# Performance work log

Hardware: AMD Instinct MI355X
Metric: run time of the kernel (lower is better)

The kernel has to match this reference:

```python
import jax, jax.numpy as jnp
import numpy as np

N = 8192
FEAT = 200
SEG = FEAT // 4  # 50
OUT = 300


def setup_inputs() -> dict:
    key = jax.random.key(0)
    ks = jax.random.split(key, 10)
    x = jax.random.normal(ks[0], (N, FEAT), dtype=jnp.float32)
    # row-normalized-ish dense adjacencies so activations stay O(1)
    A_S = jax.random.uniform(ks[1], (N, N), dtype=jnp.float32) / N
    A_F = jax.random.uniform(ks[2], (N, N), dtype=jnp.float32) / N
    gcn_W = jax.random.normal(ks[3], (SEG, SEG), dtype=jnp.float32) / np.sqrt(SEG)
    gcn_b = jnp.zeros((SEG,), dtype=jnp.float32)
    # 12 forget gates: order s1,s2,s3,f1,f2,f3,s1b,s2b,s3b,f1b,f2b,f3b
    gates_W = jax.random.normal(ks[4], (12, 2 * SEG, SEG), dtype=jnp.float32)
    gates_b = jax.random.normal(ks[5], (12, SEG), dtype=jnp.float32)
    proj_W = jax.random.normal(ks[6], (8 * SEG, OUT), dtype=jnp.float32) / np.sqrt(8 * SEG)
    proj_b = jnp.zeros((OUT,), dtype=jnp.float32)
    return {"x": x, "A_S": A_S, "A_F": A_F, "gcn_W": gcn_W, "gcn_b": gcn_b,
            "gates_W": gates_W, "gates_b": gates_b, "proj_W": proj_W, "proj_b": proj_b}


def _lgfm(x, A_S, A_F, gcn_W, gcn_b, gates_W, gates_b, proj_W, proj_b):
    seg = x.shape[1] // 4

    def gcn(h, A):
        # Kipf GraphConvolution: relu(A @ (h @ W) + b); dropout inactive (eval)
        return jax.nn.relu(A @ (h @ gcn_W) + gcn_b)

    def gate(i, h1, h2):
        a = jax.nn.sigmoid(jnp.concatenate([h1, h2], axis=1) @ gates_W[i] + gates_b[i])
        return a * h1

    GS1, GS2, GS3, GF1, GF2, GF3 = 0, 1, 2, 3, 4, 5
    GS1B, GS2B, GS3B, GF1B, GF2B, GF3B = 6, 7, 8, 9, 10, 11

    x1, x2, x3, x4 = x[:, :seg], x[:, seg:2 * seg], x[:, 2 * seg:3 * seg], x[:, 3 * seg:]

    # forward branch (F path then S gating)
    t1_XF1 = x1 + gcn(x1, A_F)
    t1_XS1 = gcn(x1, A_S)
    t1_XF2 = 0.2 * t1_XS1 + 0.8 * gcn(t1_XF1, A_F)
    t2_XF1 = x2 + gcn(x2, A_F)
    t2_XS1 = gcn(x2, A_S)
    t2_XS1 = t2_XS1 + gate(GS1, t1_XS1, t2_XS1)
    t2_XF2 = 0.2 * t2_XS1 + 0.8 * gcn(t2_XF1, A_F)
    t2_XF2 = gate(GF1, t1_XF2, t2_XF2) + t2_XF2
    t3_XF1 = 0.2 * x3 + 0.8 * gcn(x3, A_F)
    t3_XS1 = gcn(x3, A_S)
    t3_XS1 = t3_XS1 + gate(GS2, t2_XS1, t3_XS1)
    t3_XF2 = 0.2 * t3_XS1 + 0.8 * gcn(t3_XF1, A_F)
    t3_XF2 = gate(GF2, t2_XF2, t3_XF2) + t3_XF2
    t4_XF1 = x4 + gcn(x4, A_F)
    t4_XS1 = gcn(x4, A_S)
    t4_XS1 = t4_XS1 + gate(GS3, t3_XS1, t4_XS1)
    t4_XF2 = 0.2 * t4_XS1 + 0.8 * gcn(t4_XF1, A_F)
    t4_XF2 = gate(GF3, t3_XF2, t4_XF2) + t4_XF2

    # mirrored branch (S path then F gating)
    t1_XS1b = x1 + gcn(x1, A_S)
    t1_XF1b = gcn(x1, A_F)
    t1_XS2 = 0.2 * t1_XF1b + 0.8 * gcn(t1_XS1b, A_S)
    t2_XS1b = x2 + gcn(x2, A_S)
    t2_XF1b = gcn(x2, A_F)
    t2_XF1b = t2_XF1b + gate(GF1B, t1_XF1b, t2_XF1b)
    t2_XS2 = 0.2 * t2_XF1b + 0.8 * gcn(t2_XS1b, A_S)
    t2_XS2 = gate(GS1B, t1_XS2, t2_XS2) + t2_XS2
    t3_XS1b = 0.2 * x3 + 0.8 * gcn(x3, A_S)
    t3_XF1b = gcn(x3, A_F)
    t3_XF1b = t3_XF1b + gate(GF2B, t2_XF1b, t3_XF1b)
    t3_XS2 = 0.2 * t3_XF1b + 0.8 * gcn(t3_XS1b, A_S)
    t3_XS2 = gate(GS2B, t2_XS2, t3_XS2) + t3_XS2
    t4_XS1b = x4 + gcn(x4, A_S)
    t4_XF1b = gcn(x4, A_F)
    t4_XF1b = t4_XF1b + gate(GF3B, t3_XF1b, t4_XF1b)
    t4_XS2 = 0.2 * t4_XF1b + 0.8 * gcn(t4_XS1b, A_S)
    t4_XS2 = gate(GS3B, t3_XS2, t4_XS2) + t4_XS2

    h_L = jnp.concatenate([t1_XF2, t1_XS2, t2_XF2, t2_XS2,
                           t3_XF2, t3_XS2, t4_XF2, t4_XS2], axis=1)
    return h_L @ proj_W + proj_b


def reference(x, A_S, A_F, gcn_W, gcn_b, gates_W, gates_b, proj_W, proj_b):
    return _lgfm(x, A_S, A_F, gcn_W, gcn_b, gates_W, gates_b, proj_W, proj_b)
```

## Files before the change

kernel.cpp:

```cpp
#include <hip/hip_runtime.h>
#include <math.h>

typedef float float4v __attribute__((ext_vector_type(4)));
typedef __attribute__((ext_vector_type(4))) float f32x4;
typedef __attribute__((ext_vector_type(8))) short short8v;
typedef __attribute__((ext_vector_type(8))) unsigned short ushort8v;

#define NROW 8192
#define FEAT 200
#define OUTC 300
#define ZLD  256
#define HLK  448
#define HLN  384

__device__ __forceinline__ unsigned short f2bf(float x) {
  unsigned u = __float_as_uint(x);
  return (unsigned short)((u + 0x7fffu + ((u >> 16) & 1u)) >> 16);
}

__global__ __launch_bounds__(256) void zmul_t_kernel(
    const float* __restrict__ x, const float* __restrict__ W,
    unsigned short* __restrict__ Zt) {
  __shared__ float Ws[2500];
  __shared__ float hs[16][200];
  __shared__ float zbuf[16][256];
  int t = threadIdx.x;
  int r0 = blockIdx.x * 16;
  for (int i = t; i < 2500; i += 256) Ws[i] = W[i];
  for (int i = t; i < 16 * FEAT; i += 256)
    hs[0][i] = x[(size_t)r0 * FEAT + i];
  __syncthreads();
  for (int i = t; i < 16 * 256; i += 256) {
    int row = i >> 8, j = i & 255;
    float acc = 0.f;
    if (j < FEAT) {
      int s = j / 50, jj = j % 50;
      const float* hrow = &hs[row][s * 50];
      #pragma unroll 5
      for (int k = 0; k < 50; ++k) acc += hrow[k] * Ws[k * 50 + jj];
    }
    zbuf[row][j] = acc;
  }
  __syncthreads();
  unsigned int* Ztu = (unsigned int*)Zt;
  for (int i = t; i < 256 * 8; i += 256) {
    int j = i >> 3, w2 = i & 7;
    unsigned int lo = f2bf(zbuf[2 * w2][j]);
    unsigned int hi = f2bf(zbuf[2 * w2 + 1][j]);
    Ztu[((j * NROW + r0) >> 1) + w2] = lo | (hi << 16);
  }
}

__global__ __launch_bounds__(256, 2) void gemm_cvt_spill_kernel(
    const float* __restrict__ AF, const float* __restrict__ AS,
    const unsigned short* __restrict__ ZtF,
    const unsigned short* __restrict__ ZtS,
    float* __restrict__ Cpart,
    unsigned short* __restrict__ AbF_o, unsigned short* __restrict__ AbS_o) {
  int d = blockIdx.x;
  int L = (d & 7) * 64 + (d >> 3);
  int mat = L & 1;
  int ks  = (L >> 1) & 1;
  int cb  = (L >> 2) & 1;
  int rb  = L >> 3;

  const float* __restrict__ A = mat ? AS : AF;
  const unsigned short* __restrict__ Zt = mat ? ZtS : ZtF;
  unsigned short* __restrict__ Abo = mat ? AbS_o : AbF_o;

  int t = threadIdx.x;
  int lane = t & 63, wv = t >> 6;
  int row0 = rb * 128, n0 = cb * 128, k0 = ks * 4096;

  __shared__ short As[2][128 * 64];
  __shared__ short Bs[2][128 * 64];

  int srcAf[4], dstA[4];
  #pragma unroll
  for (int i = 0; i < 4; ++i) {
    int cc = i * 256 + t;
    int m = cc >> 3, s = cc & 7;
    srcAf[i] = (row0 + m) * NROW + s * 8;
    dstA[i] = m * 64 + ((s ^ (m & 7)) * 8);
  }
  int srcB[4], ldsDstB[4];
  #pragma unroll
  for (int i = 0; i < 4; ++i) {
    int c = i * 256 + t;
    int m = c >> 3, sl = c & 7;
    srcB[i] = (n0 + m) * NROW + ((sl ^ (m & 7)) * 8);
    ldsDstB[i] = (i * 256 + wv * 64) * 8;
  }

  f32x4 ar0[4], ar1[4];

#define STAGE_B(buf, kt)                                                              \
  {                                                                                   \
    _Pragma("unroll")                                                                 \
    for (int i = 0; i < 4; ++i)                                                       \
      __builtin_amdgcn_global_load_lds(                                               \
          (const __attribute__((address_space(1))) void*)(Zt + srcB[i] + (kt)),       \
          (__attribute__((address_space(3))) void*)(&Bs[buf][ldsDstB[i]]), 16, 0, 0); \
  }
#define LOAD_A(kt)                                         \
  {                                                        \
    _Pragma("unroll")                                      \
    for (int i = 0; i < 4; ++i) {                          \
      ar0[i] = *(const f32x4*)&A[srcAf[i] + (kt)];         \
      ar1[i] = *(const f32x4*)&A[srcAf[i] + (kt) + 4];     \
    }                                                      \
  }
#define WRITE_A(buf, kt)                                                                \
  {                                                                                     \
    _Pragma("unroll")                                                                   \
    for (int i = 0; i < 4; ++i) {                                                       \
      unsigned u0_, u1_, u2_, u3_;                                                      \
      asm("v_cvt_pk_bf16_f32 %0, %1, %2" : "=v"(u0_) : "v"(ar0[i][0]), "v"(ar0[i][1]));\
      asm("v_cvt_pk_bf16_f32 %0, %1, %2" : "=v"(u1_) : "v"(ar0[i][2]), "v"(ar0[i][3]));\
      asm("v_cvt_pk_bf16_f32 %0, %1, %2" : "=v"(u2_) : "v"(ar1[i][0]), "v"(ar1[i][1]));\
      asm("v_cvt_pk_bf16_f32 %0, %1, %2" : "=v"(u3_) : "v"(ar1[i][2]), "v"(ar1[i][3]));\
      union { unsigned u[4]; short8v v; } pk_;                                          \
      pk_.u[0] = u0_; pk_.u[1] = u1_; pk_.u[2] = u2_; pk_.u[3] = u3_;                   \
      *(short8v*)&As[buf][dstA[i]] = pk_.v;                                             \
      if (cb == 0) *(short8v*)&Abo[(size_t)srcAf[i] + (kt)] = pk_.v;                    \
    }                                                                                   \
  }

  f32x4 acc[4][4];
  #pragma unroll
  for (int i = 0; i < 4; ++i)
    #pragma unroll
    for (int j = 0; j < 4; ++j) acc[i][j] = (f32x4)0.f;

  int m0 = (wv >> 1) * 64, n0w = (wv & 1) * 64;
  int l15 = lane & 15, l4 = lane >> 4;

  int cur = 0;
  LOAD_A(k0)
  STAGE_B(0, k0)
  WRITE_A(0, k0)
  __syncthreads();

  for (int it = 0; it < 64; ++it) {
    if (it + 1 < 64) {
      STAGE_B(cur ^ 1, k0 + (it + 1) * 64)
      LOAD_A(k0 + (it + 1) * 64)
    }

    #pragma unroll
    for (int kk = 0; kk < 2; ++kk) {
      int slot = kk * 4 + l4;
      short8v a[4], b[4];
      #pragma unroll
      for (int i = 0; i < 4; ++i) {
        int m = m0 + i * 16 + l15;
        a[i] = *(const short8v*)&As[cur][m * 64 + ((slot ^ (m & 7)) * 8)];
        int n = n0w + i * 16 + l15;
        b[i] = *(const short8v*)&Bs[cur][n * 64 + ((slot ^ (n & 7)) * 8)];
      }
      #pragma unroll
      for (int i = 0; i < 4; ++i)
        #pragma unroll
        for (int j = 0; j < 4; ++j)
          acc[i][j] = __builtin_amdgcn_mfma_f32_16x16x32_bf16(a[i], b[j], acc[i][j], 0, 0, 0);
    }

    if (it + 1 < 64) WRITE_A(cur ^ 1, k0 + (it + 1) * 64)
    __syncthreads();
    cur ^= 1;
  }
#undef STAGE_B
#undef LOAD_A
#undef WRITE_A

  int s = mat * 2 + ks;
  #pragma unroll
  for (int i = 0; i < 4; ++i) {
    #pragma unroll
    for (int j = 0; j < 4; ++j) {
      int c = n0 + n0w + j * 16 + l15;
      #pragma unroll
      for (int q = 0; q < 4; ++q) {
        int r = row0 + m0 + i * 16 + l4 * 4 + q;
        Cpart[((size_t)(s * NROW + r) << 8) + c] = acc[i][j][q];
      }
    }
  }
}

__global__ __launch_bounds__(256, 2) void gemm_pair_kernel(
    const unsigned short* __restrict__ AbF,
    const unsigned short* __restrict__ AbS,
    const unsigned short* __restrict__ ZtF,
    const unsigned short* __restrict__ ZtS,
    float* __restrict__ Cpart) {
  int d = blockIdx.x;
  int L = (d & 7) * 64 + (d >> 3);
  int mat = L & 1;
  int ks  = (L >> 1) & 1;
  int cb  = (L >> 2) & 1;
  int rb  = L >> 3;

  const unsigned short* __restrict__ Ab = mat ? AbS : AbF;
  const unsigned short* __restrict__ Zt = mat ? ZtS : ZtF;

  int t = threadIdx.x;
  int lane = t & 63, wv = t >> 6;
  int row0 = rb * 128, n0 = cb * 128, k0 = ks * 4096;

  __shared__ short As[2][128 * 64];
  __shared__ short Bs[2][128 * 64];

  int srcA[4], srcB[4], ldsDst[4];
  #pragma unroll
  for (int i = 0; i < 4; ++i) {
    int c = i * 256 + t;
    int m = c >> 3, sl = c & 7;
    int sw = ((sl ^ (m & 7)) * 8);
    srcA[i] = (row0 + m) * NROW + sw;
    srcB[i] = (n0 + m) * NROW + sw;
    ldsDst[i] = (i * 256 + wv * 64) * 8;
  }

#define STAGE_TILE(buf, kt)                                                          \
  {                                                                                  \
    _Pragma("unroll")                                                                \
    for (int i = 0; i < 4; ++i) {                                                    \
      __builtin_amdgcn_global_load_lds(                                              \
          (const __attribute__((address_space(1))) void*)(Ab + srcA[i] + (kt)),      \
          (__attribute__((address_space(3))) void*)(&As[buf][ldsDst[i]]), 16, 0, 0); \
      __builtin_amdgcn_global_load_lds(                                              \
          (const __attribute__((address_space(1))) void*)(Zt + srcB[i] + (kt)),      \
          (__attribute__((address_space(3))) void*)(&Bs[buf][ldsDst[i]]), 16, 0, 0); \
    }                                                                                \
  }

  f32x4 acc[4][4];
  #pragma unroll
  for (int i = 0; i < 4; ++i)
    #pragma unroll
    for (int j = 0; j < 4; ++j) acc[i][j] = (f32x4)0.f;

  int m0 = (wv >> 1) * 64, n0w = (wv & 1) * 64;
  int l15 = lane & 15, l4 = lane >> 4;

  int cur = 0;
  STAGE_TILE(0, k0)
  __syncthreads();

  for (int it = 0; it < 64; ++it) {
    if (it + 1 < 64) STAGE_TILE(cur ^ 1, k0 + (it + 1) * 64)

    #pragma unroll
    for (int kk = 0; kk < 2; ++kk) {
      int slot = kk * 4 + l4;
      short8v a[4], b[4];
      #pragma unroll
      for (int i = 0; i < 4; ++i) {
        int m = m0 + i * 16 + l15;
        a[i] = *(const short8v*)&As[cur][m * 64 + ((slot ^ (m & 7)) * 8)];
        int n = n0w + i * 16 + l15;
        b[i] = *(const short8v*)&Bs[cur][n * 64 + ((slot ^ (n & 7)) * 8)];
      }
      #pragma unroll
      for (int i = 0; i < 4; ++i)
        #pragma unroll
        for (int j = 0; j < 4; ++j)
          acc[i][j] = __builtin_amdgcn_mfma_f32_16x16x32_bf16(a[i], b[j], acc[i][j], 0, 0, 0);
    }
    __syncthreads();
    cur ^= 1;
  }
#undef STAGE_TILE

  int s = mat * 2 + ks;
  #pragma unroll
  for (int i = 0; i < 4; ++i) {
    #pragma unroll
    for (int j = 0; j < 4; ++j) {
      int c = n0 + n0w + j * 16 + l15;
      #pragma unroll
      for (int q = 0; q < 4; ++q) {
        int r = row0 + m0 + i * 16 + l4 * 4 + q;
        Cpart[((size_t)(s * NROW + r) << 8) + c] = acc[i][j][q];
      }
    }
  }
}

__global__ __launch_bounds__(256) void reduce_zmul_kernel(
    const float* __restrict__ Cpart, const float* __restrict__ bias,
    const float* __restrict__ x, const float* __restrict__ W,
    float* __restrict__ GF0, float* __restrict__ GS0,
    unsigned short* __restrict__ ZtF, unsigned short* __restrict__ ZtS) {
  __shared__ float Ws[2500];
  __shared__ float hs[16][200];
  __shared__ float zbuf[16][256];
  int t = threadIdx.x;
  int r0 = blockIdx.x * 16;
  int w = t >> 6, j = t & 63;
  bool act = j < 50;
  int rbase = r0 + w * 4;
  for (int i = t; i < 2500; i += 256) Ws[i] = W[i];

  const float alpha[4] = {1.f, 1.f, 0.2f, 1.f};
  const float beta[4]  = {1.f, 1.f, 0.8f, 1.f};
  float gf[4][4], gs[4][4];
  if (act) {
    float bv = bias[j];
    #pragma unroll
    for (int r = 0; r < 4; ++r)
      #pragma unroll
      for (int s = 0; s < 4; ++s) {
        int c = s * 50 + j;
        size_t base = (((size_t)(rbase + r)) << 8) + c;
        float vF = Cpart[base] + Cpart[base + (size_t)NROW * 256];
        float vS = Cpart[base + (size_t)2 * NROW * 256] + Cpart[base + (size_t)3 * NROW * 256];
        gf[r][s] = fmaxf(vF + bv, 0.f);
        gs[r][s] = fmaxf(vS + bv, 0.f);
        GF0[(size_t)(rbase + r) * FEAT + c] = gf[r][s];
        GS0[(size_t)(rbase + r) * FEAT + c] = gs[r][s];
      }
    #pragma unroll
    for (int r = 0; r < 4; ++r)
      #pragma unroll
      for (int s = 0; s < 4; ++s)
        hs[w * 4 + r][s * 50 + j] =
            alpha[s] * x[(size_t)(rbase + r) * FEAT + s * 50 + j] + beta[s] * gf[r][s];
  }
  __syncthreads();
  for (int i = t; i < 16 * 256; i += 256) {
    int row = i >> 8, jj = i & 255;
    float acc = 0.f;
    if (jj < FEAT) {
      int s = jj / 50, j2 = jj % 50;
      const float* hrow = &hs[row][s * 50];
      #pragma unroll 5
      for (int k = 0; k < 50; ++k) acc += hrow[k] * Ws[k * 50 + j2];
    }
    zbuf[row][jj] = acc;
  }
  __syncthreads();
  {
    unsigned int* Ztu = (unsigned int*)ZtF;
    for (int i = t; i < 256 * 8; i += 256) {
      int j2 = i >> 3, w2 = i & 7;
      unsigned int lo = f2bf(zbuf[2 * w2][j2]);
      unsigned int hi = f2bf(zbuf[2 * w2 + 1][j2]);
      Ztu[((j2 * NROW + r0) >> 1) + w2] = lo | (hi << 16);
    }
  }
  if (act) {
    #pragma unroll
    for (int r = 0; r < 4; ++r)
      #pragma unroll
      for (int s = 0; s < 4; ++s)
        hs[w * 4 + r][s * 50 + j] =
            alpha[s] * x[(size_t)(rbase + r) * FEAT + s * 50 + j] + beta[s] * gs[r][s];
  }
  __syncthreads();
  for (int i = t; i < 16 * 256; i += 256) {
    int row = i >> 8, jj = i & 255;
    float acc = 0.f;
    if (jj < FEAT) {
      int s = jj / 50, j2 = jj % 50;
      const float* hrow = &hs[row][s * 50];
      #pragma unroll 5
      for (int k = 0; k < 50; ++k) acc += hrow[k] * Ws[k * 50 + j2];
    }
    zbuf[row][jj] = acc;
  }
  __syncthreads();
  {
    unsigned int* Ztu = (unsigned int*)ZtS;
    for (int i = t; i < 256 * 8; i += 256) {
      int j2 = i >> 3, w2 = i & 7;
      unsigned int lo = f2bf(zbuf[2 * w2][j2]);
      unsigned int hi = f2bf(zbuf[2 * w2 + 1][j2]);
      Ztu[((j2 * NROW + r0) >> 1) + w2] = lo | (hi << 16);
    }
  }
}

__device__ __forceinline__ void gate4(const float* __restrict__ gWi, const float* __restrict__ gbi,
                                      float* hsw, float* Wg, int t, int j, bool act,
                                      const float* h1, const float* h2, float* aout) {
  if (act) {
    #pragma unroll
    for (int r = 0; r < 4; ++r) { hsw[r * 128 + j] = h1[r]; hsw[r * 128 + 64 + j] = h2[r]; }
  }
  {
    const float4v* src = (const float4v*)gWi;
    float4v* dst = (float4v*)Wg;
    #pragma unroll
    for (int u = 0; u < 5; ++u) {
      int i = t + 256 * u;
      if (i < 1250) dst[i] = src[i];
    }
  }
  __syncthreads();
  float acc0 = 0.f, acc1 = 0.f, acc2 = 0.f, acc3 = 0.f;
  if (act) {
    float bv = gbi[j];
    acc0 = bv; acc1 = bv; acc2 = bv; acc3 = bv;
    #pragma unroll 2
    for (int k = 0; k < 50; ++k) {
      float wv = Wg[k * 50 + j];
      acc0 += hsw[0 * 128 + k] * wv;
      acc1 += hsw[1 * 128 + k] * wv;
      acc2 += hsw[2 * 128 + k] * wv;
      acc3 += hsw[3 * 128 + k] * wv;
    }
    #pragma unroll 2
    for (int k = 0; k < 50; ++k) {
      float wv = Wg[(50 + k) * 50 + j];
      acc0 += hsw[0 * 128 + 64 + k] * wv;
      acc1 += hsw[1 * 128 + 64 + k] * wv;
      acc2 += hsw[2 * 128 + 64 + k] * wv;
      acc3 += hsw[3 * 128 + 64 + k] * wv;
    }
  }
  __syncthreads();
  float accs[4] = {acc0, acc1, acc2, acc3};
  #pragma unroll
  for (int r = 0; r < 4; ++r) {
    float a = 1.f / (1.f + expf(-accs[r]));
    aout[r] = a * h1[r];
  }
}

__global__ __launch_bounds__(256) void reduce_chain_kernel(
    const float* __restrict__ Cpart, const float* __restrict__ bias,
    const float* __restrict__ GF0, const float* __restrict__ GS0,
    const float* __restrict__ gW, const float* __restrict__ gb,
    unsigned short* __restrict__ hLb) {
  __shared__ float hsb[4 * 512];
  __shared__ float Wg[5000];
  int t = threadIdx.x;
  int w = t >> 6, j = t & 63;
  bool act = j < 50;
  float* hsw = &hsb[w * 512];
  int rbase = blockIdx.x * 16 + w * 4;

  float gf0[4][4], gs0[4][4], gf1[4][4], gs1[4][4];
  if (act) {
    float bv = bias[j];
    #pragma unroll
    for (int r = 0; r < 4; ++r)
      #pragma unroll
      for (int s = 0; s < 4; ++s) {
        int c = s * 50 + j;
        size_t base = (((size_t)(rbase + r)) << 8) + c;
        float vF = Cpart[base] + Cpart[base + (size_t)NROW * 256];
        float vS = Cpart[base + (size_t)2 * NROW * 256] + Cpart[base + (size_t)3 * NROW * 256];
        gf1[r][s] = fmaxf(vF + bv, 0.f);
        gs1[r][s] = fmaxf(vS + bv, 0.f);
        gf0[r][s] = GF0[(size_t)(rbase + r) * FEAT + c];
        gs0[r][s] = GS0[(size_t)(rbase + r) * FEAT + c];
      }
  }
  if (!act) {
    for (int p = j - 50; p < 48; p += 14)
      #pragma unroll
      for (int r = 0; r < 4; ++r)
        hLb[(size_t)(rbase + r) * HLK + 400 + p] = 0;
  }

  float xf2[4], xs1[4], pre[4], a[4], h1t[4], h2t[4];
  #pragma unroll
  for (int r = 0; r < 4; ++r) xf2[r] = 0.2f * gs0[r][0] + 0.8f * gf1[r][0];
  if (act) {
    #pragma unroll
    for (int r = 0; r < 4; ++r) hLb[(size_t)(rbase + r) * HLK + 0 + j] = f2bf(xf2[r]);
  }
  #pragma unroll
  for (int r = 0; r < 4; ++r) { h1t[r] = gs0[r][0]; h2t[r] = gs0[r][1]; }
  gate4(gW + 0 * 5000, gb + 0 * 50, hsw, Wg, t, j, act, h1t, h2t, a);
  #pragma unroll
  for (int r = 0; r < 4; ++r) xs1[r] = gs0[r][1] + a[r];
  #pragma unroll
  for (int r = 0; r < 4; ++r) pre[r] = 0.2f * xs1[r] + 0.8f * gf1[r][1];
  gate4(gW + 3 * 5000, gb + 3 * 50, hsw, Wg, t, j, act, xf2, pre, a);
  #pragma unroll
  for (int r = 0; r < 4; ++r) xf2[r] = a[r] + pre[r];
  if (act) {
    #pragma unroll
    for (int r = 0; r < 4; ++r) hLb[(size_t)(rbase + r) * HLK + 100 + j] = f2bf(xf2[r]);
  }
  #pragma unroll
  for (int r = 0; r < 4; ++r) { h1t[r] = xs1[r]; h2t[r] = gs0[r][2]; }
  gate4(gW + 1 * 5000, gb + 1 * 50, hsw, Wg, t, j, act, h1t, h2t, a);
  #pragma unroll
  for (int r = 0; r < 4; ++r) xs1[r] = gs0[r][2] + a[r];
  #pragma unroll
  for (int r = 0; r < 4; ++r) pre[r] = 0.2f * xs1[r] + 0.8f * gf1[r][2];
  gate4(gW + 4 * 5000, gb + 4 * 50, hsw, Wg, t, j, act, xf2, pre, a);
  #pragma unroll
  for (int r = 0; r < 4; ++r) xf2[r] = a[r] + pre[r];
  if (act) {
    #pragma unroll
    for (int r = 0; r < 4; ++r) hLb[(size_t)(rbase + r) * HLK + 200 + j] = f2bf(xf2[r]);
  }
  #pragma unroll
  for (int r = 0; r < 4; ++r) { h1t[r] = xs1[r]; h2t[r] = gs0[r][3]; }
  gate4(gW + 2 * 5000, gb + 2 * 50, hsw, Wg, t, j, act, h1t, h2t, a);
  #pragma unroll
  for (int r = 0; r < 4; ++r) xs1[r] = gs0[r][3] + a[r];
  #pragma unroll
  for (int r = 0; r < 4; ++r) pre[r] = 0.2f * xs1[r] + 0.8f * gf1[r][3];
  gate4(gW + 5 * 5000, gb + 5 * 50, hsw, Wg, t, j, act, xf2, pre, a);
  #pragma unroll
  for (int r = 0; r < 4; ++r) xf2[r] = a[r] + pre[r];
  if (act) {
    #pragma unroll
    for (int r = 0; r < 4; ++r) hLb[(size_t)(rbase + r) * HLK + 300 + j] = f2bf(xf2[r]);
  }

  float xs2[4], xf1b[4];
  #pragma unroll
  for (int r = 0; r < 4; ++r) xs2[r] = 0.2f * gf0[r][0] + 0.8f * gs1[r][0];
  if (act) {
    #pragma unroll
    for (int r = 0; r < 4; ++r) hLb[(size_t)(rbase + r) * HLK + 50 + j] = f2bf(xs2[r]);
  }
  #pragma unroll
  for (int r = 0; r < 4; ++r) { h1t[r] = gf0[r][0]; h2t[r] = gf0[r][1]; }
  gate4(gW + 9 * 5000, gb + 9 * 50, hsw, Wg, t, j, act, h1t, h2t, a);
  #pragma unroll
  for (int r = 0; r < 4; ++r) xf1b[r] = gf0[r][1] + a[r];
  #pragma unroll
  for (int r = 0; r < 4; ++r) pre[r] = 0.2f * xf1b[r] + 0.8f * gs1[r][1];
  gate4(gW + 6 * 5000, gb + 6 * 50, hsw, Wg, t, j, act, xs2, pre, a);
  #pragma unroll
  for (int r = 0; r < 4; ++r) xs2[r] = a[r] + pre[r];
  if (act) {
    #pragma unroll
    for (int r = 0; r < 4; ++r) hLb[(size_t)(rbase + r) * HLK + 150 + j] = f2bf(xs2[r]);
  }
  #pragma unroll
  for (int r = 0; r < 4; ++r) { h1t[r] = xf1b[r]; h2t[r] = gf0[r][2]; }
  gate4(gW + 10 * 5000, gb + 10 * 50, hsw, Wg, t, j, act, h1t, h2t, a);
  #pragma unroll
  for (int r = 0; r < 4; ++r) xf1b[r] = gf0[r][2] + a[r];
  #pragma unroll
  for (int r = 0; r < 4; ++r) pre[r] = 0.2f * xf1b[r] + 0.8f * gs1[r][2];
  gate4(gW + 7 * 5000, gb + 7 * 50, hsw, Wg, t, j, act, xs2, pre, a);
  #pragma unroll
  for (int r = 0; r < 4; ++r) xs2[r] = a[r] + pre[r];
  if (act) {
    #pragma unroll
    for (int r = 0; r < 4; ++r) hLb[(size_t)(rbase + r) * HLK + 250 + j] = f2bf(xs2[r]);
  }
  #pragma unroll
  for (int r = 0; r < 4; ++r) { h1t[r] = xf1b[r]; h2t[r] = gf0[r][3]; }
  gate4(gW + 11 * 5000, gb + 11 * 50, hsw, Wg, t, j, act, h1t, h2t, a);
  #pragma unroll
  for (int r = 0; r < 4; ++r) xf1b[r] = gf0[r][3] + a[r];
  #pragma unroll
  for (int r = 0; r < 4; ++r) pre[r] = 0.2f * xf1b[r] + 0.8f * gs1[r][3];
  gate4(gW + 8 * 5000, gb + 8 * 50, hsw, Wg, t, j, act, xs2, pre, a);
  #pragma unroll
  for (int r = 0; r < 4; ++r) xs2[r] = a[r] + pre[r];
  if (act) {
    #pragma unroll
    for (int r = 0; r < 4; ++r) hLb[(size_t)(rbase + r) * HLK + 350 + j] = f2bf(xs2[r]);
  }
}

__global__ __launch_bounds__(256) void wconv_kernel(
    const float* __restrict__ pW, unsigned short* __restrict__ Wtb) {
  int i = blockIdx.x * 256 + threadIdx.x;
  if (i >= HLN * HLK) return;
  int n = i / HLK, k = i % HLK;
  float v = (n < OUTC && k < 400) ? pW[k * OUTC + n] : 0.f;
  Wtb[i] = f2bf(v);
}

__global__ __launch_bounds__(256, 2) void proj_gemm_kernel(
    const unsigned short* __restrict__ hLb,
    const unsigned short* __restrict__ Wtb,
    const float* __restrict__ pb, float* __restrict__ outp) {
  int d = blockIdx.x;
  int L = (d & 7) * 24 + (d >> 3);
  int rb = L / 3, cb = L % 3;

  int t = threadIdx.x;
  int lane = t & 63, wv = t >> 6;
  int row0 = rb * 128, n0 = cb * 128;

  __shared__ short As[2][128 * 64];
  __shared__ short Bs[2][128 * 64];

  int srcA[4], srcB[4], ldsDst[4];
  #pragma unroll
  for (int i = 0; i < 4; ++i) {
    int c = i * 256 + t;
    int m = c >> 3, sl = c & 7;
    int sw = ((sl ^ (m & 7)) * 8);
    srcA[i] = (row0 + m) * HLK + sw;
    srcB[i] = (n0 + m) * HLK + sw;
    ldsDst[i] = (i * 256 + wv * 64) * 8;
  }

#define STAGE_TILE(buf, kt)                                                          \
  {                                                                                  \
    _Pragma("unroll")                                                                \
    for (int i = 0; i < 4; ++i) {                                                    \
      __builtin_amdgcn_global_load_lds(                                              \
          (const __attribute__((address_space(1))) void*)(hLb + srcA[i] + (kt)),     \
          (__attribute__((address_space(3))) void*)(&As[buf][ldsDst[i]]), 16, 0, 0); \
      __builtin_amdgcn_global_load_lds(                                              \
          (const __attribute__((address_space(1))) void*)(Wtb + srcB[i] + (kt)),     \
          (__attribute__((address_space(3))) void*)(&Bs[buf][ldsDst[i]]), 16, 0, 0); \
    }                                                                                \
  }

  f32x4 acc[4][4];
  #pragma unroll
  for (int i = 0; i < 4; ++i)
    #pragma unroll
    for (int j = 0; j < 4; ++j) acc[i][j] = (f32x4)0.f;

  int m0 = (wv >> 1) * 64, n0w = (wv & 1) * 64;
  int l15 = lane & 15, l4 = lane >> 4;

  int cur = 0;
  STAGE_TILE(0, 0)
  __syncthreads();

  for (int it = 0; it < 7; ++it) {
    if (it + 1 < 7) STAGE_TILE(cur ^ 1, (it + 1) * 64)

    #pragma unroll
    for (int kk = 0; kk < 2; ++kk) {
      int slot = kk * 4 + l4;
      short8v a[4], b[4];
      #pragma unroll
      for (int i = 0; i < 4; ++i) {
        int m = m0 + i * 16 + l15;
        a[i] = *(const short8v*)&As[cur][m * 64 + ((slot ^ (m & 7)) * 8)];
        int n = n0w + i * 16 + l15;
        b[i] = *(const short8v*)&Bs[cur][n * 64 + ((slot ^ (n & 7)) * 8)];
      }
      #pragma unroll
      for (int i = 0; i < 4; ++i)
        #pragma unroll
        for (int j = 0; j < 4; ++j)
          acc[i][j] = __builtin_amdgcn_mfma_f32_16x16x32_bf16(a[i], b[j], acc[i][j], 0, 0, 0);
    }
    __syncthreads();
    cur ^= 1;
  }
#undef STAGE_TILE

  #pragma unroll
  for (int i = 0; i < 4; ++i) {
    #pragma unroll
    for (int j = 0; j < 4; ++j) {
      int c = n0 + n0w + j * 16 + l15;
      if (c < OUTC) {
        float b = pb[c];
        #pragma unroll
        for (int q = 0; q < 4; ++q) {
          int r = row0 + m0 + i * 16 + l4 * 4 + q;
          outp[(size_t)r * OUTC + c] = acc[i][j][q] + b;
        }
      }
    }
  }
}

__global__ __launch_bounds__(256) void zmul_f32_kernel(
    const float* __restrict__ x, const float* __restrict__ g,
    const float* __restrict__ W,
    float a0, float a1, float a2, float a3,
    float b0, float b1, float b2, float b3,
    float* __restrict__ Zp) {
  __shared__ float Ws[2500];
  __shared__ float hs[200];
  int t = threadIdx.x;
  for (int i = t; i < 2500; i += 256) Ws[i] = W[i];
  float alpha[4] = {a0, a1, a2, a3};
  float beta[4]  = {b0, b1, b2, b3};
  int s  = (t < 200) ? (t / 50) : 0;
  int jj = (t < 200) ? (t % 50) : 0;
  int r0 = blockIdx.x * 32;
  for (int rr = 0; rr < 32; ++rr) {
    int row = r0 + rr;
    __syncthreads();
    if (t < 200) hs[t] = alpha[s] * x[row * FEAT + t] + beta[s] * g[row * FEAT + t];
    __syncthreads();
    float acc = 0.f;
    if (t < 200) {
      const float* hrow = &hs[s * 50];
      #pragma unroll 5
      for (int k = 0; k < 50; ++k) acc += hrow[k] * Ws[k * 50 + jj];
    }
    Zp[row * ZLD + t] = (t < 200) ? acc : 0.f;
  }
}

#define BM 64
#define BN 64
#define BK 32
#define ALD 68
__global__ __launch_bounds__(256) void gemm_relu_kernel(
    const float* __restrict__ A, const float* __restrict__ Zp,
    const float* __restrict__ bias, float* __restrict__ C) {
  int wg  = blockIdx.x;
  int swz = (wg & 7) * 64 + (wg >> 3);
  int rb  = swz >> 2;
  int cb  = swz & 3;
  int t   = threadIdx.x;
  int rt  = t >> 4, ct = t & 15;
  __shared__ __align__(16) float As[BK][ALD];
  __shared__ __align__(16) float Zs[BK][BN];
  float acc[4][4];
  #pragma unroll
  for (int i = 0; i < 4; ++i)
    #pragma unroll
    for (int j = 0; j < 4; ++j) acc[i][j] = 0.f;
  const int row0 = rb * BM, col0 = cb * BN;
  int ar = t >> 3;
  int ak = (t & 7) * 4;
  int zr = t >> 4;
  int zc = (t & 15) * 4;
  const float4v* A4 = (const float4v*)A;
  const float4v* Z4 = (const float4v*)Zp;
  float4v a0, a1, z0, z1;
  a0 = A4[((size_t)(row0 + ar) * NROW + 0 + ak) >> 2];
  a1 = A4[((size_t)(row0 + ar + 32) * NROW + 0 + ak) >> 2];
  z0 = Z4[((0 + zr) * ZLD + col0 + zc) >> 2];
  z1 = Z4[((0 + zr + 16) * ZLD + col0 + zc) >> 2];
  for (int kt = 0; kt < NROW; kt += BK) {
    __syncthreads();
    #pragma unroll
    for (int u = 0; u < 4; ++u) As[ak + u][ar] = a0[u];
    #pragma unroll
    for (int u = 0; u < 4; ++u) As[ak + u][ar + 32] = a1[u];
    *(float4v*)&Zs[zr][zc]      = z0;
    *(float4v*)&Zs[zr + 16][zc] = z1;
    __syncthreads();
    int kn = kt + BK;
    if (kn < NROW) {
      a0 = A4[((size_t)(row0 + ar) * NROW + kn + ak) >> 2];
      a1 = A4[((size_t)(row0 + ar + 32) * NROW + kn + ak) >> 2];
      z0 = Z4[((kn + zr) * ZLD + col0 + zc) >> 2];
      z1 = Z4[((kn + zr + 16) * ZLD + col0 + zc) >> 2];
    }
    #pragma unroll
    for (int k = 0; k < BK; ++k) {
      float4v av = *(const float4v*)&As[k][rt * 4];
      float4v zv = *(const float4v*)&Zs[k][ct * 4];
      #pragma unroll
      for (int i = 0; i < 4; ++i)
        #pragma unroll
        for (int j = 0; j < 4; ++j) acc[i][j] += av[i] * zv[j];
    }
  }
  #pragma unroll
  for (int i = 0; i < 4; ++i) {
    int grow = row0 + rt * 4 + i;
    #pragma unroll
    for (int j = 0; j < 4; ++j) {
      int gcol = col0 + ct * 4 + j;
      if (gcol < FEAT) {
        float v = acc[i][j] + bias[gcol % 50];
        C[(size_t)grow * FEAT + gcol] = fmaxf(v, 0.f);
      }
    }
  }
}

__global__ __launch_bounds__(256) void chain_top_kernel(
    const float* __restrict__ GS0, const float* __restrict__ GF1,
    const float* __restrict__ gW, const float* __restrict__ gb,
    unsigned short* __restrict__ hLb) {
  __shared__ float hsb[4 * 512];
  __shared__ float Wg[5000];
  int t = threadIdx.x;
  int w = t >> 6, j = t & 63;
  bool act = j < 50;
  float* hsw = &hsb[w * 512];
  int rbase = blockIdx.x * 16 + w * 4;
  float gs[4][4], gf[4][4];
  #pragma unroll
  for (int r = 0; r < 4; ++r)
    #pragma unroll
    for (int s = 0; s < 4; ++s) { gs[r][s] = 0.f; gf[r][s] = 0.f; }
  if (act) {
    #pragma unroll
    for (int r = 0; r < 4; ++r)
      #pragma unroll
      for (int s = 0; s < 4; ++s) {
        gs[r][s] = GS0[(size_t)(rbase + r) * FEAT + s * 50 + j];
        gf[r][s] = GF1[(size_t)(rbase + r) * FEAT + s * 50 + j];
      }
  }
  float xf2[4], xs1[4], pre[4], a[4], h1t[4], h2t[4];
  #pragma unroll
  for (int r = 0; r < 4; ++r) xf2[r] = 0.2f * gs[r][0] + 0.8f * gf[r][0];
  if (act) {
    #pragma unroll
    for (int r = 0; r < 4; ++r) hLb[(size_t)(rbase + r) * HLK + 0 + j] = f2bf(xf2[r]);
  }
  #pragma unroll
  for (int r = 0; r < 4; ++r) { h1t[r] = gs[r][0]; h2t[r] = gs[r][1]; }
  gate4(gW + 0 * 5000, gb + 0 * 50, hsw, Wg, t, j, act, h1t, h2t, a);
  #pragma unroll
  for (int r = 0; r < 4; ++r) xs1[r] = gs[r][1] + a[r];
  #pragma unroll
  for (int r = 0; r < 4; ++r) pre[r] = 0.2f * xs1[r] + 0.8f * gf[r][1];
  gate4(gW + 3 * 5000, gb + 3 * 50, hsw, Wg, t, j, act, xf2, pre, a);
  #pragma unroll
  for (int r = 0; r < 4; ++r) xf2[r] = a[r] + pre[r];
  if (act) {
    #pragma unroll
    for (int r = 0; r < 4; ++r) hLb[(size_t)(rbase + r) * HLK + 100 + j] = f2bf(xf2[r]);
  }
  #pragma unroll
  for (int r = 0; r < 4; ++r) { h1t[r] = xs1[r]; h2t[r] = gs[r][2]; }
  gate4(gW + 1 * 5000, gb + 1 * 50, hsw, Wg, t, j, act, h1t, h2t, a);
  #pragma unroll
  for (int r = 0; r < 4; ++r) xs1[r] = gs[r][2] + a[r];
  #pragma unroll
  for (int r = 0; r < 4; ++r) pre[r] = 0.2f * xs1[r] + 0.8f * gf[r][2];
  gate4(gW + 4 * 5000, gb + 4 * 50, hsw, Wg, t, j, act, xf2, pre, a);
  #pragma unroll
  for (int r = 0; r < 4; ++r) xf2[r] = a[r] + pre[r];
  if (act) {
    #pragma unroll
    for (int r = 0; r < 4; ++r) hLb[(size_t)(rbase + r) * HLK + 200 + j] = f2bf(xf2[r]);
  }
  #pragma unroll
  for (int r = 0; r < 4; ++r) { h1t[r] = xs1[r]; h2t[r] = gs[r][3]; }
  gate4(gW + 2 * 5000, gb + 2 * 50, hsw, Wg, t, j, act, h1t, h2t, a);
  #pragma unroll
  for (int r = 0; r < 4; ++r) xs1[r] = gs[r][3] + a[r];
  #pragma unroll
  for (int r = 0; r < 4; ++r) pre[r] = 0.2f * xs1[r] + 0.8f * gf[r][3];
  gate4(gW + 5 * 5000, gb + 5 * 50, hsw, Wg, t, j, act, xf2, pre, a);
  #pragma unroll
  for (int r = 0; r < 4; ++r) xf2[r] = a[r] + pre[r];
  if (act) {
    #pragma unroll
    for (int r = 0; r < 4; ++r) hLb[(size_t)(rbase + r) * HLK + 300 + j] = f2bf(xf2[r]);
  }
}

__global__ __launch_bounds__(256) void chain_bottom_kernel(
    const float* __restrict__ GF0, const float* __restrict__ GS1,
    const float* __restrict__ gW, const float* __restrict__ gb,
    unsigned short* __restrict__ hLb) {
  __shared__ float hsb[4 * 512];
  __shared__ float Wg[5000];
  int t = threadIdx.x;
  int w = t >> 6, j = t & 63;
  bool act = j < 50;
  float* hsw = &hsb[w * 512];
  int rbase = blockIdx.x * 16 + w * 4;
  float gf0[4][4], gs1[4][4];
  #pragma unroll
  for (int r = 0; r < 4; ++r)
    #pragma unroll
    for (int s = 0; s < 4; ++s) { gf0[r][s] = 0.f; gs1[r][s] = 0.f; }
  if (act) {
    #pragma unroll
    for (int r = 0; r < 4; ++r)
      #pragma unroll
      for (int s = 0; s < 4; ++s) {
        gf0[r][s] = GF0[(size_t)(rbase + r) * FEAT + s * 50 + j];
        gs1[r][s] = GS1[(size_t)(rbase + r) * FEAT + s * 50 + j];
      }
  }
  float xs2[4], xf1b[4], pre[4], a[4], h1t[4], h2t[4];
  #pragma unroll
  for (int r = 0; r < 4; ++r) xs2[r] = 0.2f * gf0[r][0] + 0.8f * gs1[r][0];
  if (act) {
    #pragma unroll
    for (int r = 0; r < 4; ++r) hLb[(size_t)(rbase + r) * HLK + 50 + j] = f2bf(xs2[r]);
  }
  #pragma unroll
  for (int r = 0; r < 4; ++r) { h1t[r] = gf0[r][0]; h2t[r] = gf0[r][1]; }
  gate4(gW + 9 * 5000, gb + 9 * 50, hsw, Wg, t, j, act, h1t, h2t, a);
  #pragma unroll
  for (int r = 0; r < 4; ++r) xf1b[r] = gf0[r][1] + a[r];
  #pragma unroll
  for (int r = 0; r < 4; ++r) pre[r] = 0.2f * xf1b[r] + 0.8f * gs1[r][1];
  gate4(gW + 6 * 5000, gb + 6 * 50, hsw, Wg, t, j, act, xs2, pre, a);
  #pragma unroll
  for (int r = 0; r < 4; ++r) xs2[r] = a[r] + pre[r];
  if (act) {
    #pragma unroll
    for (int r = 0; r < 4; ++r) hLb[(size_t)(rbase + r) * HLK + 150 + j] = f2bf(xs2[r]);
  }
  #pragma unroll
  for (int r = 0; r < 4; ++r) { h1t[r] = xf1b[r]; h2t[r] = gf0[r][2]; }
  gate4(gW + 10 * 5000, gb + 10 * 50, hsw, Wg, t, j, act, h1t, h2t, a);
  #pragma unroll
  for (int r = 0; r < 4; ++r) xf1b[r] = gf0[r][2] + a[r];
  #pragma unroll
  for (int r = 0; r < 4; ++r) pre[r] = 0.2f * xf1b[r] + 0.8f * gs1[r][2];
  gate4(gW + 7 * 5000, gb + 7 * 50, hsw, Wg, t, j, act, xs2, pre, a);
  #pragma unroll
  for (int r = 0; r < 4; ++r) xs2[r] = a[r] + pre[r];
  if (act) {
    #pragma unroll
    for (int r = 0; r < 4; ++r) hLb[(size_t)(rbase + r) * HLK + 250 + j] = f2bf(xs2[r]);
  }
  #pragma unroll
  for (int r = 0; r < 4; ++r) { h1t[r] = xf1b[r]; h2t[r] = gf0[r][3]; }
  gate4(gW + 11 * 5000, gb + 11 * 50, hsw, Wg, t, j, act, h1t, h2t, a);
  #pragma unroll
  for (int r = 0; r < 4; ++r) xf1b[r] = gf0[r][3] + a[r];
  #pragma unroll
  for (int r = 0; r < 4; ++r) pre[r] = 0.2f * xf1b[r] + 0.8f * gs1[r][3];
  gate4(gW + 8 * 5000, gb + 8 * 50, hsw, Wg, t, j, act, xs2, pre, a);
  #pragma unroll
  for (int r = 0; r < 4; ++r) xs2[r] = a[r] + pre[r];
  if (act) {
    #pragma unroll
    for (int r = 0; r < 4; ++r) hLb[(size_t)(rbase + r) * HLK + 350 + j] = f2bf(xs2[r]);
  }
}

extern "C" void kernel_launch(void* const* d_in, const int* in_sizes, int n_in,
                              void* d_out, int out_size, void* d_ws, size_t ws_size,
                              hipStream_t stream) {
  const float* x       = (const float*)d_in[0];
  const float* A_S     = (const float*)d_in[1];
  const float* A_F     = (const float*)d_in[2];
  const float* gcn_W   = (const float*)d_in[3];
  const float* gcn_b   = (const float*)d_in[4];
  const float* gates_W = (const float*)d_in[5];
  const float* gates_b = (const float*)d_in[6];
  const float* proj_W  = (const float*)d_in[7];
  const float* proj_b  = (const float*)d_in[8];
  float* out = (float*)d_out;

  const size_t szAb    = (size_t)NROW * NROW * 2;
  const size_t szZt    = (size_t)256 * NROW * 2;
  const size_t szCpart = (size_t)4 * NROW * 256 * 4;
  const size_t szG     = (size_t)NROW * FEAT * 4;
  const size_t szHLb   = (size_t)NROW * HLK * 2;
  const size_t szWtb   = (size_t)HLN * HLK * 2;
  const size_t need = 2 * szAb + 3 * szZt + szCpart + 2 * szG + szHLb + szWtb;

  if (ws_size >= need) {
    char* w = (char*)d_ws;
    unsigned short* AbF  = (unsigned short*)w;           w += szAb;
    unsigned short* AbS  = (unsigned short*)w;           w += szAb;
    unsigned short* Zt0  = (unsigned short*)w;           w += szZt;
    unsigned short* Zt1F = (unsigned short*)w;           w += szZt;
    unsigned short* Zt1S = (unsigned short*)w;           w += szZt;
    float* Cpart = (float*)w;                            w += szCpart;
    float* GF0 = (float*)w;                              w += szG;
    float* GS0 = (float*)w;                              w += szG;
    unsigned short* hLb = (unsigned short*)w;            w += szHLb;
    unsigned short* Wtb = (unsigned short*)w;

    wconv_kernel<<<(HLN * HLK + 255) / 256, 256, 0, stream>>>(proj_W, Wtb);
    zmul_t_kernel<<<512, 256, 0, stream>>>(x, gcn_W, Zt0);

    gemm_cvt_spill_kernel<<<512, 256, 0, stream>>>(A_F, A_S, Zt0, Zt0, Cpart, AbF, AbS);
    reduce_zmul_kernel<<<512, 256, 0, stream>>>(Cpart, gcn_b, x, gcn_W, GF0, GS0, Zt1F, Zt1S);

    gemm_pair_kernel<<<512, 256, 0, stream>>>(AbF, AbS, Zt1F, Zt1S, Cpart);
    reduce_chain_kernel<<<512, 256, 0, stream>>>(Cpart, gcn_b, GF0, GS0, gates_W, gates_b, hLb);

    proj_gemm_kernel<<<192, 256, 0, stream>>>(hLb, Wtb, proj_b, out);
  } else {
    char* w = (char*)d_ws;
    float* Z   = (float*)w;                              w += (size_t)NROW * ZLD * 4;
    float* GF0 = (float*)w;                              w += szG;
    float* GS0 = (float*)w;                              w += szG;
    float* GF1 = (float*)w;                              w += szG;
    float* GS1 = (float*)w;                              w += szG;
    unsigned short* hLb = (unsigned short*)w;            w += szHLb;
    unsigned short* Wtb = (unsigned short*)w;

    hipMemsetAsync(hLb, 0, szHLb, stream);
    wconv_kernel<<<(HLN * HLK + 255) / 256, 256, 0, stream>>>(proj_W, Wtb);

    zmul_f32_kernel<<<256, 256, 0, stream>>>(x, x, gcn_W, 1.f, 1.f, 1.f, 1.f, 0.f, 0.f, 0.f, 0.f, Z);
    gemm_relu_kernel<<<512, 256, 0, stream>>>(A_F, Z, gcn_b, GF0);
    gemm_relu_kernel<<<512, 256, 0, stream>>>(A_S, Z, gcn_b, GS0);
    zmul_f32_kernel<<<256, 256, 0, stream>>>(x, GF0, gcn_W, 1.f, 1.f, 0.2f, 1.f, 1.f, 1.f, 0.8f, 1.f, Z);
    gemm_relu_kernel<<<512, 256, 0, stream>>>(A_F, Z, gcn_b, GF1);
    zmul_f32_kernel<<<256, 256, 0, stream>>>(x, GS0, gcn_W, 1.f, 1.f, 0.2f, 1.f, 1.f, 1.f, 0.8f, 1.f, Z);
    gemm_relu_kernel<<<512, 256, 0, stream>>>(A_S, Z, gcn_b, GS1);

    chain_top_kernel<<<512, 256, 0, stream>>>(GS0, GF1, gates_W, gates_b, hLb);
    chain_bottom_kernel<<<512, 256, 0, stream>>>(GF0, GS1, gates_W, gates_b, hLb);
    proj_gemm_kernel<<<192, 256, 0, stream>>>(hLb, Wtb, proj_b, out);
  }
}
```

Measured before the change: 481.3 us.

## Prefetch fp32 A two tiles ahead and split bf16 spill writes across column blocks

Adds a second register bank for the fp32 adjacency tile so global loads are issued two iterations ahead instead of one, giving more latency slack before the convert-and-write to LDS. The loop is manually unrolled by two with fixed LDS buffer indices. The bf16 copy of A written back to global memory is now shared between column blocks (cb 0 writes the first half of K, cb 1 the second half) rather than done entirely by cb 0, which balances store traffic. The extra register bank raises VGPR pressure, which may affect occupancy under the launch bounds.

```diff
diff --git a/kernel.cpp b/kernel.cpp
--- a/kernel.cpp
+++ b/kernel.cpp
@@ -92,7 +92,7 @@
     ldsDstB[i] = (i * 256 + wv * 64) * 8;
   }
 
-  f32x4 ar0[4], ar1[4];
+  f32x4 aA0[4], aA1[4], aB0[4], aB1[4];
 
 #define STAGE_B(buf, kt)                                                              \
   {                                                                                   \
@@ -102,29 +102,48 @@
           (const __attribute__((address_space(1))) void*)(Zt + srcB[i] + (kt)),       \
           (__attribute__((address_space(3))) void*)(&Bs[buf][ldsDstB[i]]), 16, 0, 0); \
   }
-#define LOAD_A(kt)                                         \
+#define LOAD_BANK(b0, b1, kt)                              \
   {                                                        \
     _Pragma("unroll")                                      \
     for (int i = 0; i < 4; ++i) {                          \
-      ar0[i] = *(const f32x4*)&A[srcAf[i] + (kt)];         \
-      ar1[i] = *(const f32x4*)&A[srcAf[i] + (kt) + 4];     \
+      b0[i] = *(const f32x4*)&A[srcAf[i] + (kt)];          \
+      b1[i] = *(const f32x4*)&A[srcAf[i] + (kt) + 4];      \
     }                                                      \
   }
-#define WRITE_A(buf, kt)                                                                \
+#define WRITE_BANK(buf, b0, b1, kt, spill)                                              \
   {                                                                                     \
     _Pragma("unroll")                                                                   \
     for (int i = 0; i < 4; ++i) {                                                       \
       unsigned u0_, u1_, u2_, u3_;                                                      \
-      asm("v_cvt_pk_bf16_f32 %0, %1, %2" : "=v"(u0_) : "v"(ar0[i][0]), "v"(ar0[i][1]));\
-      asm("v_cvt_pk_bf16_f32 %0, %1, %2" : "=v"(u1_) : "v"(ar0[i][2]), "v"(ar0[i][3]));\
-      asm("v_cvt_pk_bf16_f32 %0, %1, %2" : "=v"(u2_) : "v"(ar1[i][0]), "v"(ar1[i][1]));\
-      asm("v_cvt_pk_bf16_f32 %0, %1, %2" : "=v"(u3_) : "v"(ar1[i][2]), "v"(ar1[i][3]));\
+      asm("v_cvt_pk_bf16_f32 %0, %1, %2" : "=v"(u0_) : "v"(b0[i][0]), "v"(b0[i][1]));   \
+      asm("v_cvt_pk_bf16_f32 %0, %1, %2" : "=v"(u1_) : "v"(b0[i][2]), "v"(b0[i][3]));   \
+      asm("v_cvt_pk_bf16_f32 %0, %1, %2" : "=v"(u2_) : "v"(b1[i][0]), "v"(b1[i][1]));   \
+      asm("v_cvt_pk_bf16_f32 %0, %1, %2" : "=v"(u3_) : "v"(b1[i][2]), "v"(b1[i][3]));   \
       union { unsigned u[4]; short8v v; } pk_;                                          \
       pk_.u[0] = u0_; pk_.u[1] = u1_; pk_.u[2] = u2_; pk_.u[3] = u3_;                   \
       *(short8v*)&As[buf][dstA[i]] = pk_.v;                                             \
-      if (cb == 0) *(short8v*)&Abo[(size_t)srcAf[i] + (kt)] = pk_.v;                    \
+      if (spill) *(short8v*)&Abo[(size_t)srcAf[i] + (kt)] = pk_.v;                      \
     }                                                                                   \
   }
+#define MFMA_TILE(buf)                                                                  \
+  {                                                                                     \
+    _Pragma("unroll")                                                                   \
+    for (int kk = 0; kk < 2; ++kk) {                                                    \
+      int slot = kk * 4 + l4;                                                           \
+      short8v a[4], b[4];                                                               \
+      _Pragma("unroll")                                                                 \
+      for (int i = 0; i < 4; ++i) {                                                     \
+        int m = m0 + i * 16 + l15;                                                      \
+        a[i] = *(const short8v*)&As[buf][m * 64 + ((slot ^ (m & 7)) * 8)];              \
+        int n = n0w + i * 16 + l15;                                                     \
+        b[i] = *(const short8v*)&Bs[buf][n * 64 + ((slot ^ (n & 7)) * 8)];              \
+      }                                                                                 \
+      _Pragma("unroll")                                                                 \
+      for (int i = 0; i < 4; ++i)                                                       \
+        _Pragma("unroll")                                                               \
+        for (int j = 0; j < 4; ++j)                                                     \
+          acc[i][j] = __builtin_amdgcn_mfma_f32_16x16x32_bf16(a[i], b[j], acc[i][j], 0, 0, 0); \
+  } }
 
   f32x4 acc[4][4];
   #pragma unroll
@@ -135,43 +154,40 @@
   int m0 = (wv >> 1) * 64, n0w = (wv & 1) * 64;
   int l15 = lane & 15, l4 = lane >> 4;
 
-  int cur = 0;
-  LOAD_A(k0)
+  LOAD_BANK(aA0, aA1, k0)
+  LOAD_BANK(aB0, aB1, k0 + 64)
   STAGE_B(0, k0)
-  WRITE_A(0, k0)
+  WRITE_BANK(0, aA0, aA1, k0, (cb == 0))
   __syncthreads();
 
-  for (int it = 0; it < 64; ++it) {
-    if (it + 1 < 64) {
-      STAGE_B(cur ^ 1, k0 + (it + 1) * 64)
-      LOAD_A(k0 + (it + 1) * 64)
-    }
-
-    #pragma unroll
-    for (int kk = 0; kk < 2; ++kk) {
-      int slot = kk * 4 + l4;
-      short8v a[4], b[4];
-      #pragma unroll
-      for (int i = 0; i < 4; ++i) {
-        int m = m0 + i * 16 + l15;
-        a[i] = *(const short8v*)&As[cur][m * 64 + ((slot ^ (m & 7)) * 8)];
-        int n = n0w + i * 16 + l15;
-        b[i] = *(const short8v*)&Bs[cur][n * 64 + ((slot ^ (n & 7)) * 8)];
-      }
-      #pragma unroll
-      for (int i = 0; i < 4; ++i)
-        #pragma unroll
-        for (int j = 0; j < 4; ++j)
-          acc[i][j] = __builtin_amdgcn_mfma_f32_16x16x32_bf16(a[i], b[j], acc[i][j], 0, 0, 0);
-    }
-
-    if (it + 1 < 64) WRITE_A(cur ^ 1, k0 + (it + 1) * 64)
-    __syncthreads();
-    cur ^= 1;
+  for (int itp = 0; itp < 32; ++itp) {
+    {
+      int it = 2 * itp;
+      if (it + 1 < 64) STAGE_B(1, k0 + (it + 1) * 64)
+      if (it + 2 < 64) LOAD_BANK(aA0, aA1, k0 + (it + 2) * 64)
+      MFMA_TILE(0)
+      if (it + 1 < 64) {
+        bool sp = (cb == ((it + 1) >= 32 ? 1 : 0));
+        WRITE_BANK(1, aB0, aB1, k0 + (it + 1) * 64, sp)
+      }
+      __syncthreads();
+    }
+    {
+      int it = 2 * itp + 1;
+      if (it + 1 < 64) STAGE_B(0, k0 + (it + 1) * 64)
+      if (it + 2 < 64) LOAD_BANK(aB0, aB1, k0 + (it + 2) * 64)
+      MFMA_TILE(1)
+      if (it + 1 < 64) {
+        bool sp = (cb == ((it + 1) >= 32 ? 1 : 0));
+        WRITE_BANK(0, aA0, aA1, k0 + (it + 1) * 64, sp)
+      }
+      __syncthreads();
+    }
   }
 #undef STAGE_B
-#undef LOAD_A
-#undef WRITE_A
+#undef LOAD_BANK
+#undef WRITE_BANK
+#undef MFMA_TILE
 
   int s = mat * 2 + ks;
   #pragma unroll
```

After: 485.6 us. About the same (+0.9%).
